# Kernel tuning notes

Hardware: AMD Instinct MI355X
Metric: run time of the kernel (lower is better)

Reference implementation:

```python
import jax, jax.numpy as jnp
import numpy as np

T, INPUT, POP_EXC, POP_INH = 128, 2048, 2048, 512
DT = 1e-3
TAU_SYN_INV, TAU_MEM_INV = 200.0, 100.0
V_LEAK, V_TH, V_RESET = 0.0, 1.0, 0.0
RHO_RESET = 5.0            # refractory counter reset (in steps)
ALPHA = 100.0              # SuperSpike surrogate slope (used in bwd variant)
A_PRE = A_POST = 1.0
TAU_PRE_INV = TAU_POST_INV = 50.0
ETA_PLUS = ETA_MINUS = 1e-3
W_MIN, W_MAX = 0.0, 1.0


def heaviside(x):
    return (x > 0).astype(x.dtype)


def lif_refrac_step(inp, v, i, rho):
    # norse LIF feed-forward step
    v_dec = v + DT * TAU_MEM_INV * ((V_LEAK - v) + i)
    i_dec = i * (1.0 - DT * TAU_SYN_INV)
    z = heaviside(v_dec - V_TH)
    v_new = (1.0 - z) * v_dec + z * V_RESET
    i_new = i_dec + inp
    # refractory update
    refrac = heaviside(rho)                      # neurons still refractory
    v_new = (1.0 - refrac) * v_new + refrac * V_RESET
    z = (1.0 - refrac) * z
    rho_new = (1.0 - z) * jax.nn.relu(rho - refrac) + z * RHO_RESET
    return z, v_new, i_new, rho_new


def stdp_step(z_pre, z_post, w, t_pre, t_post):
    # additive STDP (norse stdp_step_linear, mu=0) with trace low-pass filters
    t_pre = t_pre + DT * TAU_PRE_INV * (-t_pre + A_PRE * z_pre)
    t_post = t_post + DT * TAU_POST_INV * (-t_post + A_POST * z_post)
    dw = ETA_PLUS * jnp.outer(z_post, t_pre) - ETA_MINUS * jnp.outer(t_post, z_pre)
    w = jnp.clip(w + dw, W_MIN, W_MAX)           # (post, pre)
    return w, t_pre, t_post


def setup_inputs() -> dict:
    key = jax.random.key(0)
    k1, k2, k3 = jax.random.split(key, 3)
    exc_currents = 2.0 * jax.random.uniform(k1, (T, INPUT), dtype=jnp.float32)
    w_exc = 0.05 * jax.random.uniform(k2, (POP_EXC, INPUT), dtype=jnp.float32)
    w_inh = 0.05 * jax.random.uniform(k3, (POP_INH, POP_EXC), dtype=jnp.float32)
    return {"exc_currents": exc_currents, "w_exc": w_exc, "w_inh": w_inh}


def reference(exc_currents, w_exc, w_inh):
    zf = jnp.zeros
    carry0 = (
        w_exc, zf(POP_EXC), zf(POP_EXC), zf(POP_EXC),   # w, v, i, rho (exc)
        zf(INPUT), zf(POP_EXC),                         # t_pre, t_post (exc)
        w_inh, zf(POP_INH), zf(POP_INH), zf(POP_INH),   # w, v, i, rho (inh)
        zf(POP_EXC), zf(POP_INH),                       # t_pre, t_post (inh)
    )

    def step(c, x):
        (we, ve, ie, re, tpe, tqe, wi, vi, ii, ri, tpi, tqi) = c
        # excitatory STDP layer: matvec input current, LIF-refrac, STDP update
        z_e, ve, ie, re = lif_refrac_step(x @ we.T, ve, ie, re)
        we, tpe, tqe = stdp_step(x, z_e, we, tpe, tqe)
        # inhibitory STDP layer driven by excitatory spikes
        z_i, vi, ii, ri = lif_refrac_step(z_e @ wi.T, vi, ii, ri)
        wi, tpi, tqi = stdp_step(z_e, z_i, wi, tpi, tqi)
        return (we, ve, ie, re, tpe, tqe, wi, vi, ii, ri, tpi, tqi), z_e

    _, spikes = jax.lax.scan(step, carry0, exc_currents)
    return spikes  # [T, POP_EXC]
```

## Files before the change

### kernel.cpp

```cpp
#include <hip/hip_runtime.h>


constexpr int T_STEPS = 128;
constexpr int N_IN    = 2048;
constexpr int N_EXC   = 2048;

__global__ __launch_bounds__(256)
void tp_precompute_kernel(const float* __restrict__ x, float* __restrict__ tp_ws) {
    const int j = blockIdx.x * blockDim.x + threadIdx.x;
    float tp = 0.f;
    #pragma unroll 4
    for (int t = 0; t < T_STEPS; ++t) {
        tp = fmaf(0.05f, x[t * N_IN + j] - tp, tp);
        tp_ws[t * N_IN + j] = tp;
    }
}

template <int CTRL, int RM>
__device__ __forceinline__ float dpp_add(float x) {
    int t = __builtin_amdgcn_update_dpp(0, __builtin_bit_cast(int, x),
                                        CTRL, RM, 0xF, true);
    return x + __builtin_bit_cast(float, t);
}

__device__ __forceinline__ float wave_sum64(float x) {
    x = dpp_add<0x111, 0xF>(x);
    x = dpp_add<0x112, 0xF>(x);
    x = dpp_add<0x114, 0xF>(x);
    x = dpp_add<0x118, 0xF>(x);
    x = dpp_add<0x142, 0xA>(x);
    x = dpp_add<0x143, 0xC>(x);
    return __builtin_bit_cast(float,
        __builtin_amdgcn_readlane(__builtin_bit_cast(int, x), 63));
}

__device__ __forceinline__ float clamp01(float x) {
    return __builtin_amdgcn_fmed3f(x, 0.f, 1.f);
}

__global__ __launch_bounds__(256, 2)
void snn_exc_kernel(const float* __restrict__ x,
                    const float* __restrict__ w0,
                    const float* __restrict__ tp_ws,
                    float* __restrict__ out)
{
    const int lane = threadIdx.x & 63;
    const int wid  = threadIdx.x >> 6;
    const int row  = blockIdx.x * 4 + wid;

    float w[32];
    {
        const float4* wrow = reinterpret_cast<const float4*>(w0 + (size_t)row * N_IN);
        #pragma unroll
        for (int m = 0; m < 8; ++m) {
            float4 t4 = wrow[m * 64 + lane];
            w[4*m+0] = t4.x; w[4*m+1] = t4.y; w[4*m+2] = t4.z; w[4*m+3] = t4.w;
        }
    }

    const float4* xbase = reinterpret_cast<const float4*>(x) + lane;
    const float4* tpb   = reinterpret_cast<const float4*>(tp_ws) + lane;
    float*        outp  = out + row;

    float4 xa[8], xb[8];
    #pragma unroll
    for (int m = 0; m < 8; ++m) xa[m] = xbase[m * 64];

    const float4* xpf = xbase + (N_IN / 4);

    float v = 0.f, syn = 0.f, rho = 0.f, tpost = 0.f;

    auto step = [&](int t, bool pf, const float4 (&xc)[8], float4 (&xn)[8]) {
        if (pf) {
            #pragma unroll
            for (int m = 0; m < 8; ++m) xn[m] = xpf[m * 64];
        }
        xpf += N_IN / 4;

        const float v_dec = fmaf(0.1f, syn - v, v);
        const bool refrac = (rho > 0.f);
        const bool spike  = (v_dec > 1.0f) && !refrac;
        v   = (spike || refrac) ? 0.f : v_dec;
        rho = spike ? 5.0f : fmaxf(rho - 1.0f, 0.f);
        const float zf = spike ? 1.f : 0.f;
        tpost = fmaf(0.05f, zf - tpost, tpost);
        const float c2 = 1e-3f * tpost;
        if (lane == 0) *outp = zf;
        outp += N_EXC;

        float4 tq[8];
        if (spike) {
            const float4* tq4 = tpb + (size_t)t * (N_IN / 4);
            #pragma unroll
            for (int m = 0; m < 8; ++m) tq[m] = tq4[m * 64];
        }

        float a0 = 0.f, a1 = 0.f, a2 = 0.f, a3 = 0.f;
        #pragma unroll
        for (int m = 0; m < 8; ++m) {
            a0 = fmaf(xc[m].x, w[4*m+0], a0);
            a1 = fmaf(xc[m].y, w[4*m+1], a1);
            a2 = fmaf(xc[m].z, w[4*m+2], a2);
            a3 = fmaf(xc[m].w, w[4*m+3], a3);
        }

        if (spike) {
            #pragma unroll
            for (int m = 0; m < 8; ++m) {
                w[4*m+0] = clamp01(fmaf(1e-3f, tq[m].x, fmaf(-c2, xc[m].x, w[4*m+0])));
                w[4*m+1] = clamp01(fmaf(1e-3f, tq[m].y, fmaf(-c2, xc[m].y, w[4*m+1])));
                w[4*m+2] = clamp01(fmaf(1e-3f, tq[m].z, fmaf(-c2, xc[m].z, w[4*m+2])));
                w[4*m+3] = clamp01(fmaf(1e-3f, tq[m].w, fmaf(-c2, xc[m].w, w[4*m+3])));
            }
        } else {
            #pragma unroll
            for (int m = 0; m < 8; ++m) {
                w[4*m+0] = clamp01(fmaf(-c2, xc[m].x, w[4*m+0]));
                w[4*m+1] = clamp01(fmaf(-c2, xc[m].y, w[4*m+1]));
                w[4*m+2] = clamp01(fmaf(-c2, xc[m].z, w[4*m+2]));
                w[4*m+3] = clamp01(fmaf(-c2, xc[m].w, w[4*m+3]));
            }
        }

        syn = fmaf(0.8f, syn, wave_sum64((a0 + a1) + (a2 + a3)));
    };

    for (int t = 0; t < T_STEPS - 2; t += 2) {
        step(t,     true, xa, xb);
        step(t + 1, true, xb, xa);
    }
    step(T_STEPS - 2, true,  xa, xb);
    step(T_STEPS - 1, false, xb, xa);

}

extern "C" void kernel_launch(void* const* d_in, const int* in_sizes, int n_in,
                              void* d_out, int out_size, void* d_ws, size_t ws_size,
                              hipStream_t stream) {
    const float* x  = (const float*)d_in[0];
    const float* w0 = (const float*)d_in[1];
    float* out = (float*)d_out;

    float* tp_ws = (float*)d_ws;
    tp_precompute_kernel<<<N_IN / 256, 256, 0, stream>>>(x, tp_ws);

    dim3 grid(N_EXC / 4);
    dim3 block(256);
    snn_exc_kernel<<<grid, block, 0, stream>>>(x, w0, tp_ws, out);
}
```

Before: 90.93 us.

## Stage input currents through shared memory shared by the block's four waves

Each block's four waves previously each loaded the full input row from global memory every step. Now the block cooperatively loads four timesteps at a time into an 8-slot LDS ring buffer, prefetching the next four into registers, and each wave reads x from LDS. This cuts redundant global/L2 traffic by four but adds a __syncthreads per four steps and 64KB of LDS, which may limit occupancy.

New measurement: 185.5 us. +104.0%, slower.

```diff
diff --git a/kernel.cpp b/kernel.cpp
--- a/kernel.cpp
+++ b/kernel.cpp
@@ -44,8 +44,11 @@
                     const float* __restrict__ tp_ws,
                     float* __restrict__ out)
 {
-    const int lane = threadIdx.x & 63;
-    const int wid  = threadIdx.x >> 6;
+    __shared__ __align__(16) float xs[8][N_IN];
+
+    const int tid  = threadIdx.x;
+    const int lane = tid & 63;
+    const int wid  = tid >> 6;
     const int row  = blockIdx.x * 4 + wid;
 
     float w[32];
@@ -58,24 +61,27 @@
         }
     }
 
-    const float4* xbase = reinterpret_cast<const float4*>(x) + lane;
-    const float4* tpb   = reinterpret_cast<const float4*>(tp_ws) + lane;
-    float*        outp  = out + row;
+    const size_t stage_off = (size_t)wid * 512 + (size_t)lane * 4;
+    const float4* tpb = reinterpret_cast<const float4*>(tp_ws) + lane;
+    float* outp = out + row;
 
-    float4 xa[8], xb[8];
+    float4 pr[8];
     #pragma unroll
-    for (int m = 0; m < 8; ++m) xa[m] = xbase[m * 64];
-
-    const float4* xpf = xbase + (N_IN / 4);
+    for (int j = 0; j < 4; ++j) {
+        const float* src = x + (size_t)j * N_IN + stage_off;
+        pr[2*j+0] = *reinterpret_cast<const float4*>(src);
+        pr[2*j+1] = *reinterpret_cast<const float4*>(src + 256);
+    }
 
     float v = 0.f, syn = 0.f, rho = 0.f, tpost = 0.f;
 
-    auto step = [&](int t, bool pf, const float4 (&xc)[8], float4 (&xn)[8]) {
-        if (pf) {
+    auto step = [&](int t) {
+        float4 xq[8];
+        {
+            const float4* xl = reinterpret_cast<const float4*>(xs[t & 7]);
             #pragma unroll
-            for (int m = 0; m < 8; ++m) xn[m] = xpf[m * 64];
+            for (int m = 0; m < 8; ++m) xq[m] = xl[m * 64 + lane];
         }
-        xpf += N_IN / 4;
 
         const float v_dec = fmaf(0.1f, syn - v, v);
         const bool refrac = (rho > 0.f);
@@ -98,40 +104,54 @@
         float a0 = 0.f, a1 = 0.f, a2 = 0.f, a3 = 0.f;
         #pragma unroll
         for (int m = 0; m < 8; ++m) {
-            a0 = fmaf(xc[m].x, w[4*m+0], a0);
-            a1 = fmaf(xc[m].y, w[4*m+1], a1);
-            a2 = fmaf(xc[m].z, w[4*m+2], a2);
-            a3 = fmaf(xc[m].w, w[4*m+3], a3);
+            a0 = fmaf(xq[m].x, w[4*m+0], a0);
+            a1 = fmaf(xq[m].y, w[4*m+1], a1);
+            a2 = fmaf(xq[m].z, w[4*m+2], a2);
+            a3 = fmaf(xq[m].w, w[4*m+3], a3);
         }
 
         if (spike) {
             #pragma unroll
             for (int m = 0; m < 8; ++m) {
-                w[4*m+0] = clamp01(fmaf(1e-3f, tq[m].x, fmaf(-c2, xc[m].x, w[4*m+0])));
-                w[4*m+1] = clamp01(fmaf(1e-3f, tq[m].y, fmaf(-c2, xc[m].y, w[4*m+1])));
-                w[4*m+2] = clamp01(fmaf(1e-3f, tq[m].z, fmaf(-c2, xc[m].z, w[4*m+2])));
-                w[4*m+3] = clamp01(fmaf(1e-3f, tq[m].w, fmaf(-c2, xc[m].w, w[4*m+3])));
+                w[4*m+0] = clamp01(fmaf(1e-3f, tq[m].x, fmaf(-c2, xq[m].x, w[4*m+0])));
+                w[4*m+1] = clamp01(fmaf(1e-3f, tq[m].y, fmaf(-c2, xq[m].y, w[4*m+1])));
+                w[4*m+2] = clamp01(fmaf(1e-3f, tq[m].z, fmaf(-c2, xq[m].z, w[4*m+2])));
+                w[4*m+3] = clamp01(fmaf(1e-3f, tq[m].w, fmaf(-c2, xq[m].w, w[4*m+3])));
             }
         } else {
             #pragma unroll
             for (int m = 0; m < 8; ++m) {
-                w[4*m+0] = clamp01(fmaf(-c2, xc[m].x, w[4*m+0]));
-                w[4*m+1] = clamp01(fmaf(-c2, xc[m].y, w[4*m+1]));
-                w[4*m+2] = clamp01(fmaf(-c2, xc[m].z, w[4*m+2]));
-                w[4*m+3] = clamp01(fmaf(-c2, xc[m].w, w[4*m+3]));
+                w[4*m+0] = clamp01(fmaf(-c2, xq[m].x, w[4*m+0]));
+                w[4*m+1] = clamp01(fmaf(-c2, xq[m].y, w[4*m+1]));
+                w[4*m+2] = clamp01(fmaf(-c2, xq[m].z, w[4*m+2]));
+                w[4*m+3] = clamp01(fmaf(-c2, xq[m].w, w[4*m+3]));
             }
         }
 
         syn = fmaf(0.8f, syn, wave_sum64((a0 + a1) + (a2 + a3)));
     };
 
-    for (int t = 0; t < T_STEPS - 2; t += 2) {
-        step(t,     true, xa, xb);
-        step(t + 1, true, xb, xa);
+    for (int tb = 0; tb < T_STEPS; tb += 4) {
+        #pragma unroll
+        for (int j = 0; j < 4; ++j) {
+            float* dst = &xs[(tb + j) & 7][0] + stage_off;
+            *reinterpret_cast<float4*>(dst)       = pr[2*j+0];
+            *reinterpret_cast<float4*>(dst + 256) = pr[2*j+1];
+        }
+        __syncthreads();
+        if (tb + 4 < T_STEPS) {
+            #pragma unroll
+            for (int j = 0; j < 4; ++j) {
+                const float* src = x + (size_t)(tb + 4 + j) * N_IN + stage_off;
+                pr[2*j+0] = *reinterpret_cast<const float4*>(src);
+                pr[2*j+1] = *reinterpret_cast<const float4*>(src + 256);
+            }
+        }
+        step(tb + 0);
+        step(tb + 1);
+        step(tb + 2);
+        step(tb + 3);
     }
-    step(T_STEPS - 2, true,  xa, xb);
-    step(T_STEPS - 1, false, xb, xa);
-
 }
 
 extern "C" void kernel_launch(void* const* d_in, const int* in_sizes, int n_in,
```

## Split input dimension across waves with shared-memory partial sums per neuron group

Applied to the files above, without the earlier changes.

Each block now handles 4 neurons, with each wave owning a 512-wide slice of the input for all 4 neurons instead of one full row. The four wave partial sums go into a double-buffered shared array and are combined, with a block barrier every timestep. This cuts the per-wave x and trace loads by four and shrinks register state per thread, at the cost of one __syncthreads per step and four reductions per wave. The trace precompute loop unroll is also raised.

Measured after the change: 138.7 us. 52.5% more time.

```diff
diff --git a/kernel.cpp b/kernel.cpp
--- a/kernel.cpp
+++ b/kernel.cpp
@@ -4,12 +4,13 @@
 constexpr int T_STEPS = 128;
 constexpr int N_IN    = 2048;
 constexpr int N_EXC   = 2048;
+constexpr int SLICE   = 512;
 
 __global__ __launch_bounds__(256)
 void tp_precompute_kernel(const float* __restrict__ x, float* __restrict__ tp_ws) {
     const int j = blockIdx.x * blockDim.x + threadIdx.x;
     float tp = 0.f;
-    #pragma unroll 4
+    #pragma unroll 16
     for (int t = 0; t < T_STEPS; ++t) {
         tp = fmaf(0.05f, x[t * N_IN + j] - tp, tp);
         tp_ws[t * N_IN + j] = tp;
@@ -44,94 +45,136 @@
                     const float* __restrict__ tp_ws,
                     float* __restrict__ out)
 {
-    const int lane = threadIdx.x & 63;
-    const int wid  = threadIdx.x >> 6;
-    const int row  = blockIdx.x * 4 + wid;
+    __shared__ float part[2][4][4];
 
-    float w[32];
-    {
-        const float4* wrow = reinterpret_cast<const float4*>(w0 + (size_t)row * N_IN);
+    const int tid  = threadIdx.x;
+    const int lane = tid & 63;
+    const int wid  = tid >> 6;
+    const int nb   = blockIdx.x * 4;
+
+    float w[4][8];
+    #pragma unroll
+    for (int n = 0; n < 4; ++n) {
+        const float4* wr = reinterpret_cast<const float4*>(
+            w0 + (size_t)(nb + n) * N_IN + wid * SLICE);
         #pragma unroll
-        for (int m = 0; m < 8; ++m) {
-            float4 t4 = wrow[m * 64 + lane];
-            w[4*m+0] = t4.x; w[4*m+1] = t4.y; w[4*m+2] = t4.z; w[4*m+3] = t4.w;
+        for (int m = 0; m < 2; ++m) {
+            float4 t4 = wr[m * 64 + lane];
+            w[n][4*m+0] = t4.x; w[n][4*m+1] = t4.y;
+            w[n][4*m+2] = t4.z; w[n][4*m+3] = t4.w;
         }
     }
 
-    const float4* xbase = reinterpret_cast<const float4*>(x) + lane;
-    const float4* tpb   = reinterpret_cast<const float4*>(tp_ws) + lane;
-    float*        outp  = out + row;
+    const float4* xsl = reinterpret_cast<const float4*>(x + wid * SLICE) + lane;
+    const float4* tps = reinterpret_cast<const float4*>(tp_ws + wid * SLICE) + lane;
 
-    float4 xa[8], xb[8];
-    #pragma unroll
-    for (int m = 0; m < 8; ++m) xa[m] = xbase[m * 64];
+    if (tid < 32) reinterpret_cast<float*>(part)[tid] = 0.f;
 
-    const float4* xpf = xbase + (N_IN / 4);
+    float4 xa0 = xsl[0], xa1 = xsl[64];
+    float4 xb0 = xa0, xb1 = xa1;
+    __syncthreads();
 
-    float v = 0.f, syn = 0.f, rho = 0.f, tpost = 0.f;
+    float v[4]     = {0.f, 0.f, 0.f, 0.f};
+    float syn[4]   = {0.f, 0.f, 0.f, 0.f};
+    float rho[4]   = {0.f, 0.f, 0.f, 0.f};
+    float tpost[4] = {0.f, 0.f, 0.f, 0.f};
 
-    auto step = [&](int t, bool pf, const float4 (&xc)[8], float4 (&xn)[8]) {
-        if (pf) {
-            #pragma unroll
-            for (int m = 0; m < 8; ++m) xn[m] = xpf[m * 64];
-        }
-        xpf += N_IN / 4;
+    auto step = [&](int t, float4& xc0, float4& xc1, float4& xn0, float4& xn1) {
+        const float* pb = &part[t & 1][0][0];
+        const float4 pA = *reinterpret_cast<const float4*>(pb + 0);
+        const float4 pB = *reinterpret_cast<const float4*>(pb + 4);
+        const float4 pC = *reinterpret_cast<const float4*>(pb + 8);
+        const float4 pD = *reinterpret_cast<const float4*>(pb + 12);
 
-        const float v_dec = fmaf(0.1f, syn - v, v);
-        const bool refrac = (rho > 0.f);
-        const bool spike  = (v_dec > 1.0f) && !refrac;
-        v   = (spike || refrac) ? 0.f : v_dec;
-        rho = spike ? 5.0f : fmaxf(rho - 1.0f, 0.f);
-        const float zf = spike ? 1.f : 0.f;
-        tpost = fmaf(0.05f, zf - tpost, tpost);
-        const float c2 = 1e-3f * tpost;
-        if (lane == 0) *outp = zf;
-        outp += N_EXC;
+        int tn = t + 1; if (tn > T_STEPS - 1) tn = T_STEPS - 1;
+        const float4* xp = xsl + (size_t)tn * (N_IN / 4);
+        xn0 = xp[0]; xn1 = xp[64];
 
-        float4 tq[8];
-        if (spike) {
-            const float4* tq4 = tpb + (size_t)t * (N_IN / 4);
-            #pragma unroll
-            for (int m = 0; m < 8; ++m) tq[m] = tq4[m * 64];
+        const float totn[4] = {
+            (pA.x + pB.x) + (pC.x + pD.x),
+            (pA.y + pB.y) + (pC.y + pD.y),
+            (pA.z + pB.z) + (pC.z + pD.z),
+            (pA.w + pB.w) + (pC.w + pD.w) };
+        float z[4], c2[4];
+        int sk[4];
+        #pragma unroll
+        for (int n = 0; n < 4; ++n) {
+            syn[n] = fmaf(0.8f, syn[n], totn[n]);
+            const float vd = fmaf(0.1f, syn[n] - v[n], v[n]);
+            const bool rf = (rho[n] > 0.f);
+            const bool s  = (vd > 1.0f) && !rf;
+            v[n]   = (s || rf) ? 0.f : vd;
+            rho[n] = s ? 5.0f : fmaxf(rho[n] - 1.0f, 0.f);
+            z[n]   = s ? 1.f : 0.f;
+            tpost[n] = fmaf(0.05f, z[n] - tpost[n], tpost[n]);
+            c2[n]  = 1e-3f * tpost[n];
+            sk[n]  = __builtin_amdgcn_readfirstlane((int)s);
         }
 
-        float a0 = 0.f, a1 = 0.f, a2 = 0.f, a3 = 0.f;
-        #pragma unroll
-        for (int m = 0; m < 8; ++m) {
-            a0 = fmaf(xc[m].x, w[4*m+0], a0);
-            a1 = fmaf(xc[m].y, w[4*m+1], a1);
-            a2 = fmaf(xc[m].z, w[4*m+2], a2);
-            a3 = fmaf(xc[m].w, w[4*m+3], a3);
+        const float zsel = (wid == 0) ? z[0] : (wid == 1) ? z[1]
+                         : (wid == 2) ? z[2] : z[3];
+        if (lane == 0) out[(size_t)t * N_EXC + nb + wid] = zsel;
+
+        float4 tq0, tq1;
+        if (sk[0] | sk[1] | sk[2] | sk[3]) {
+            const float4* tp4 = tps + (size_t)t * (N_IN / 4);
+            tq0 = tp4[0]; tq1 = tp4[64];
         }
 
-        if (spike) {
-            #pragma unroll
-            for (int m = 0; m < 8; ++m) {
-                w[4*m+0] = clamp01(fmaf(1e-3f, tq[m].x, fmaf(-c2, xc[m].x, w[4*m+0])));
-                w[4*m+1] = clamp01(fmaf(1e-3f, tq[m].y, fmaf(-c2, xc[m].y, w[4*m+1])));
-                w[4*m+2] = clamp01(fmaf(1e-3f, tq[m].z, fmaf(-c2, xc[m].z, w[4*m+2])));
-                w[4*m+3] = clamp01(fmaf(1e-3f, tq[m].w, fmaf(-c2, xc[m].w, w[4*m+3])));
-            }
-        } else {
-            #pragma unroll
-            for (int m = 0; m < 8; ++m) {
-                w[4*m+0] = clamp01(fmaf(-c2, xc[m].x, w[4*m+0]));
-                w[4*m+1] = clamp01(fmaf(-c2, xc[m].y, w[4*m+1]));
-                w[4*m+2] = clamp01(fmaf(-c2, xc[m].z, w[4*m+2]));
-                w[4*m+3] = clamp01(fmaf(-c2, xc[m].w, w[4*m+3]));
+        float acc[4];
+        #pragma unroll
+        for (int n = 0; n < 4; ++n) {
+            float a =      xc0.x * w[n][0];
+            a = fmaf(xc0.y, w[n][1], a);
+            a = fmaf(xc0.z, w[n][2], a);
+            a = fmaf(xc0.w, w[n][3], a);
+            a = fmaf(xc1.x, w[n][4], a);
+            a = fmaf(xc1.y, w[n][5], a);
+            a = fmaf(xc1.z, w[n][6], a);
+            a = fmaf(xc1.w, w[n][7], a);
+            acc[n] = a;
+        }
+
+        const float r0 = wave_sum64(acc[0]);
+        const float r1 = wave_sum64(acc[1]);
+        const float r2 = wave_sum64(acc[2]);
+        const float r3 = wave_sum64(acc[3]);
+        if (lane == 0) {
+            float4 pw; pw.x = r0; pw.y = r1; pw.z = r2; pw.w = r3;
+            *reinterpret_cast<float4*>(&part[(t + 1) & 1][wid][0]) = pw;
+        }
+
+        #pragma unroll
+        for (int n = 0; n < 4; ++n) {
+            const float cc = c2[n];
+            if (sk[n]) {
+                w[n][0] = clamp01(fmaf(1e-3f, tq0.x, fmaf(-cc, xc0.x, w[n][0])));
+                w[n][1] = clamp01(fmaf(1e-3f, tq0.y, fmaf(-cc, xc0.y, w[n][1])));
+                w[n][2] = clamp01(fmaf(1e-3f, tq0.z, fmaf(-cc, xc0.z, w[n][2])));
+                w[n][3] = clamp01(fmaf(1e-3f, tq0.w, fmaf(-cc, xc0.w, w[n][3])));
+                w[n][4] = clamp01(fmaf(1e-3f, tq1.x, fmaf(-cc, xc1.x, w[n][4])));
+                w[n][5] = clamp01(fmaf(1e-3f, tq1.y, fmaf(-cc, xc1.y, w[n][5])));
+                w[n][6] = clamp01(fmaf(1e-3f, tq1.z, fmaf(-cc, xc1.z, w[n][6])));
+                w[n][7] = clamp01(fmaf(1e-3f, tq1.w, fmaf(-cc, xc1.w, w[n][7])));
+            } else {
+                w[n][0] = clamp01(fmaf(-cc, xc0.x, w[n][0]));
+                w[n][1] = clamp01(fmaf(-cc, xc0.y, w[n][1]));
+                w[n][2] = clamp01(fmaf(-cc, xc0.z, w[n][2]));
+                w[n][3] = clamp01(fmaf(-cc, xc0.w, w[n][3]));
+                w[n][4] = clamp01(fmaf(-cc, xc1.x, w[n][4]));
+                w[n][5] = clamp01(fmaf(-cc, xc1.y, w[n][5]));
+                w[n][6] = clamp01(fmaf(-cc, xc1.z, w[n][6]));
+                w[n][7] = clamp01(fmaf(-cc, xc1.w, w[n][7]));
             }
         }
 
-        syn = fmaf(0.8f, syn, wave_sum64((a0 + a1) + (a2 + a3)));
+        __syncthreads();
     };
 
-    for (int t = 0; t < T_STEPS - 2; t += 2) {
-        step(t,     true, xa, xb);
-        step(t + 1, true, xb, xa);
+    for (int t = 0; t < T_STEPS; t += 2) {
+        step(t,     xa0, xa1, xb0, xb1);
+        step(t + 1, xb0, xb1, xa0, xa1);
     }
-    step(T_STEPS - 2, true,  xa, xb);
-    step(T_STEPS - 1, false, xb, xa);
-
 }
 
 extern "C" void kernel_launch(void* const* d_in, const int* in_sizes, int n_in,
```
